# Kernel tuning notes

Hardware: AMD Instinct MI355X
Metric: run time of the kernel (lower is better)

## Reference

```python
import jax, jax.numpy as jnp
import numpy as np

B, N, D = 2, 2048, 1024
H, QH, DH = 8, 16, 64        # kv heads, query heads, head dim
SOFTCLAMP = 50.0


def setup_inputs() -> dict:
    key = jax.random.key(0)
    ks = jax.random.split(key, 7)
    return {
        "tokens": jax.random.normal(ks[0], (B, N, D), jnp.float32),
        "norm_w": jnp.ones((D,), jnp.float32) + 0.02 * jax.random.normal(ks[1], (D,), jnp.float32),
        "Wq":  0.02 * jax.random.normal(ks[2], (D, QH * DH), jnp.float32),
        "Wkv": 0.02 * jax.random.normal(ks[3], (D, 2 * H * DH), jnp.float32),
        "Wout": 0.02 * jax.random.normal(ks[4], (H * DH, D), jnp.float32),
        "q_gamma": 0.02 * jax.random.normal(ks[5], (QH, DH), jnp.float32),
        "k_gamma": 0.02 * jax.random.normal(ks[6], (H, DH), jnp.float32),
    }


def _rmsnorm(x, w):
    eps = jnp.finfo(x.dtype).eps
    return x * jax.lax.rsqrt(jnp.mean(x * x, axis=-1, keepdims=True) + eps) * w


def _l2norm(x):
    # F.normalize(dim=-1, p=2) clamps the norm at eps=1e-12
    n = jnp.maximum(jnp.linalg.norm(x, axis=-1, keepdims=True), 1e-12)
    return x / n


def _mh_rmsnorm(x, gamma):
    # x: [b, h, n, d]; gamma: [h, d]; scale = (gamma + 1) * sqrt(d)
    scale = (gamma + 1.0) * np.sqrt(x.shape[-1]).astype(np.float32)
    return _l2norm(x) * scale[None, :, None, :]


def reference(tokens, norm_w, Wq, Wkv, Wout, q_gamma, k_gamma):
    b, n, d = tokens.shape
    x = _rmsnorm(tokens, norm_w)

    q = (x @ Wq).reshape(b, n, QH, DH).transpose(0, 2, 1, 3)      # [b, QH, n, dh]
    kv = x @ Wkv
    k = kv[..., : H * DH].reshape(b, n, H, DH).transpose(0, 2, 1, 3)  # [b, H, n, dh]
    v = kv[..., H * DH:].reshape(b, n, H, DH).transpose(0, 2, 1, 3)   # [b, H, n, dh]

    q = _mh_rmsnorm(q, q_gamma)
    k = _mh_rmsnorm(k, k_gamma)

    g = QH // H
    q = q.reshape(b, H, g, n, DH)                                 # [b, h, g, i, dh]

    sim = jnp.einsum('bhgid,bhjd->bhgij', q, k)                   # [b, h, g, i, j]
    sim = jnp.tanh(sim / SOFTCLAMP) * SOFTCLAMP                   # softcap BEFORE scale (faithful)
    sim = sim * (DH ** -0.5)

    neg = -jnp.finfo(sim.dtype).max
    causal = jnp.triu(jnp.ones((n, n), dtype=bool), 1)
    sim = jnp.where(causal, neg, sim)

    attn = jax.nn.softmax(sim, axis=-1)
    # NOTE: original einsum sums over the group axis g -> [b, h, i, dh]
    out = jnp.einsum('bhgij,bhjd->bhid', attn, v)
    out = out.transpose(0, 2, 1, 3).reshape(b, n, H * DH)
    return out @ Wout
```

## Files before the change

kernel.cpp:

```cpp
#include <hip/hip_runtime.h>
#include <hip/hip_bf16.h>
#include <type_traits>

typedef unsigned short u16;
typedef __attribute__((ext_vector_type(2))) float f32x2;
typedef __attribute__((ext_vector_type(4))) float f32x4;
typedef __attribute__((ext_vector_type(8))) short short8;
typedef __attribute__((ext_vector_type(4))) short short4v;
typedef __attribute__((ext_vector_type(8))) __bf16 bf16x8;
typedef __attribute__((ext_vector_type(4))) __bf16 bf16x4;

#define BB 2
#define NN 2048
#define DDIM 1024
#define HH 8
#define QHH 16
#define DHH 64

__device__ __forceinline__ float b2f(u16 v) {
    return __builtin_bit_cast(float, ((unsigned)v) << 16);
}
__device__ __forceinline__ u16 f2b(float f) {
    unsigned u = __builtin_bit_cast(unsigned, f);
    u += 0x7FFFu + ((u >> 16) & 1u);
    return (u16)(u >> 16);
}
__device__ __forceinline__ float fastrcp(float x) {
#if __has_builtin(__builtin_amdgcn_rcpf)
    return __builtin_amdgcn_rcpf(x);
#else
    return 1.0f / x;
#endif
}
__device__ __forceinline__ float fastexp2(float x) {
#if __has_builtin(__builtin_amdgcn_exp2f)
    return __builtin_amdgcn_exp2f(x);
#else
    return exp2f(x);
#endif
}
__device__ __forceinline__ f32x2 sp2(float v) { return (f32x2){v, v}; }
__device__ __forceinline__ f32x4 mfma16(short8 a, short8 b, f32x4 c) {
    return __builtin_amdgcn_mfma_f32_16x16x32_bf16(
        __builtin_bit_cast(bf16x8, a), __builtin_bit_cast(bf16x8, b), c, 0, 0, 0);
}
#if __has_builtin(__builtin_amdgcn_mfma_f32_16x16x16_bf16)
__device__ __forceinline__ f32x4 mfma_k16(short4v a, short4v b, f32x4 c) {
    return __builtin_amdgcn_mfma_f32_16x16x16_bf16(
        __builtin_bit_cast(bf16x4, a), __builtin_bit_cast(bf16x4, b), c, 0, 0, 0);
}
#else
__device__ __forceinline__ f32x4 mfma_k16(short4v a, short4v b, f32x4 c) {
    return __builtin_amdgcn_mfma_f32_16x16x16bf16_1k(a, b, c, 0, 0, 0);
}
#endif
__device__ __forceinline__ void stage16(const u16* g, u16* l, int lane) {
#if __has_builtin(__builtin_amdgcn_global_load_lds)
    __builtin_amdgcn_global_load_lds(
        (const __attribute__((address_space(1))) unsigned int*)g,
        (__attribute__((address_space(3))) unsigned int*)l, 16, 0, 0);
#else
    *(short8*)(l + lane * 8) = *(const short8*)g;
#endif
}

__global__ __launch_bounds__(256) void k_rmsnorm(const float* __restrict__ tokens,
                                                 const float* __restrict__ norm_w,
                                                 u16* __restrict__ xb) {
    const int row = blockIdx.x;
    const int tid = threadIdx.x;
    const float* xp = tokens + (size_t)row * DDIM + tid * 4;
    float4 raw = *(const float4*)xp;
    float ss = raw.x * raw.x + raw.y * raw.y + raw.z * raw.z + raw.w * raw.w;
#pragma unroll
    for (int d = 1; d < 64; d <<= 1) ss += __shfl_xor(ss, d);
    __shared__ float red[4];
    if ((tid & 63) == 0) red[tid >> 6] = ss;
    __syncthreads();
    float tot = red[0] + red[1] + red[2] + red[3];
    float r = rsqrtf(tot * (1.0f / 1024.0f) + 1.1920929e-7f);
    float4 wv = *(const float4*)(norm_w + tid * 4);
    ushort4 o;
    o.x = f2b(raw.x * r * wv.x);
    o.y = f2b(raw.y * r * wv.y);
    o.z = f2b(raw.z * r * wv.z);
    o.w = f2b(raw.w * r * wv.w);
    *(ushort4*)(xb + (size_t)row * DDIM + tid * 4) = o;
}

__global__ __launch_bounds__(256) void k_wprep(const float* __restrict__ Wq,
                                               const float* __restrict__ Wkv,
                                               const float* __restrict__ Wout,
                                               u16* __restrict__ WqT,
                                               u16* __restrict__ WkvT,
                                               u16* __restrict__ WoutT) {
    const int z = blockIdx.z;
    const float* in = (z == 0) ? Wq : (z == 1) ? Wkv : Wout;
    u16* out = (z == 0) ? WqT : (z == 1) ? WkvT : WoutT;
    const int R = (z == 2) ? 512 : 1024, C = 1024;
    const int br = blockIdx.y * 32;
    if (br >= R) return;
    __shared__ u16 tile[32][33];
    const int bc = blockIdx.x * 32;
    const int tx = threadIdx.x & 31, ty = threadIdx.x >> 5;
#pragma unroll
    for (int i = 0; i < 32; i += 8) tile[ty + i][tx] = f2b(in[(size_t)(br + ty + i) * C + bc + tx]);
    __syncthreads();
#pragma unroll
    for (int i = 0; i < 32; i += 8) out[(size_t)(bc + ty + i) * R + br + tx] = tile[tx][ty + i];
}

__global__ __launch_bounds__(256) void k_gemm128(const u16* __restrict__ A,
                                                 const u16* __restrict__ Bt,
                                                 u16* __restrict__ C,
                                                 int M, int Ncols, int K) {
    __shared__ __attribute__((aligned(16))) u16 As[128 * 32];
    __shared__ __attribute__((aligned(16))) u16 Bs[128 * 32];
    const int tid = threadIdx.x;
    const int lane = tid & 63;
    const int w = tid >> 6;
    const int m0 = blockIdx.y * 128;
    const int n0 = blockIdx.x * 128;
    const int wr = (w >> 1) * 64;
    const int wc = (w & 1) * 64;
    const int lr = lane & 15;
    const int lq = lane >> 4;

    const int ch0 = w * 32;
    const u16* aSrc = A + (size_t)(m0 + ch0 + (lane >> 2)) * K + (lane & 3) * 8;
    const u16* bSrc = Bt + (size_t)(n0 + ch0 + (lane >> 2)) * K + (lane & 3) * 8;
    u16* aDst = As + ch0 * 32;
    u16* bDst = Bs + ch0 * 32;

    f32x4 acc[4][4];
#pragma unroll
    for (int i = 0; i < 4; i++)
#pragma unroll
        for (int j = 0; j < 4; j++) acc[i][j] = (f32x4){0.f, 0.f, 0.f, 0.f};

    for (int k0 = 0; k0 < K; k0 += 32) {
        __syncthreads();
        stage16(aSrc, aDst, lane);
        stage16(aSrc + (size_t)16 * K, aDst + 512, lane);
        stage16(bSrc, bDst, lane);
        stage16(bSrc + (size_t)16 * K, bDst + 512, lane);
        aSrc += 32;
        bSrc += 32;
        __syncthreads();
        short8 a[4], b[4];
#pragma unroll
        for (int mi = 0; mi < 4; ++mi) a[mi] = *(const short8*)&As[(wr + mi * 16 + lr) * 32 + lq * 8];
#pragma unroll
        for (int ni = 0; ni < 4; ++ni) b[ni] = *(const short8*)&Bs[(wc + ni * 16 + lr) * 32 + lq * 8];
#pragma unroll
        for (int mi = 0; mi < 4; ++mi)
#pragma unroll
            for (int ni = 0; ni < 4; ++ni) acc[mi][ni] = mfma16(a[mi], b[ni], acc[mi][ni]);
    }
#pragma unroll
    for (int mi = 0; mi < 4; ++mi)
#pragma unroll
        for (int ni = 0; ni < 4; ++ni)
#pragma unroll
            for (int r = 0; r < 4; ++r) {
                int row = m0 + wr + mi * 16 + lq * 4 + r;
                int col = n0 + wc + ni * 16 + lr;
                C[(size_t)row * Ncols + col] = f2b(acc[mi][ni][r]);
            }
}

__global__ __launch_bounds__(256) void k_gemm64f(const u16* __restrict__ A,
                                                 const u16* __restrict__ Bt,
                                                 float* __restrict__ C,
                                                 int M, int Ncols, int K) {
    __shared__ __attribute__((aligned(16))) u16 As[64 * 32];
    __shared__ __attribute__((aligned(16))) u16 Bs[128 * 32];
    const int tid = threadIdx.x;
    const int lane = tid & 63;
    const int w = tid >> 6;
    const int m0 = blockIdx.y * 64;
    const int n0 = blockIdx.x * 128;
    const int lr = lane & 15;
    const int lq = lane >> 4;

    const u16* aSrc = A + (size_t)(m0 + w * 16 + (lane >> 2)) * K + (lane & 3) * 8;
    const u16* bSrc = Bt + (size_t)(n0 + w * 32 + (lane >> 2)) * K + (lane & 3) * 8;
    u16* aDst = As + w * 16 * 32;
    u16* bDst = Bs + w * 32 * 32;

    f32x4 acc[8];
#pragma unroll
    for (int i = 0; i < 8; i++) acc[i] = (f32x4){0.f, 0.f, 0.f, 0.f};

    for (int k0 = 0; k0 < K; k0 += 32) {
        __syncthreads();
        stage16(aSrc, aDst, lane);
        stage16(bSrc, bDst, lane);
        stage16(bSrc + (size_t)16 * K, bDst + 512, lane);
        aSrc += 32;
        bSrc += 32;
        __syncthreads();
        short8 a = *(const short8*)&As[(w * 16 + lr) * 32 + lq * 8];
#pragma unroll
        for (int nt = 0; nt < 8; ++nt) {
            short8 b = *(const short8*)&Bs[(nt * 16 + lr) * 32 + lq * 8];
            acc[nt] = mfma16(a, b, acc[nt]);
        }
    }
#pragma unroll
    for (int nt = 0; nt < 8; ++nt)
#pragma unroll
        for (int r = 0; r < 4; ++r) {
            int row = m0 + w * 16 + lq * 4 + r;
            int col = n0 + nt * 16 + lr;
            C[(size_t)row * Ncols + col] = acc[nt][r];
        }
}

__global__ __launch_bounds__(256) void k_headnorm(const u16* __restrict__ qkv,
                                                  const float* __restrict__ q_gamma,
                                                  const float* __restrict__ k_gamma,
                                                  u16* __restrict__ qn,
                                                  u16* __restrict__ kn) {
    const int row = blockIdx.x;
    const int b = row >> 11, n = row & 2047;
    const int lane = threadIdx.x & 63, w = threadIdx.x >> 6;
    const u16* qr = qkv + (size_t)row * 2048;
    const u16* kvr = qkv + (size_t)row * 2048 + 1024;
#pragma unroll
    for (int t = 0; t < 4; ++t) {
        int qh = w * 4 + t;
        float v = b2f(qr[qh * 64 + lane]);
        float ss = v * v;
#pragma unroll
        for (int d = 1; d < 64; d <<= 1) ss += __shfl_xor(ss, d);
        float nrm = fmaxf(sqrtf(ss), 1e-12f);
        float g = q_gamma[qh * 64 + lane];
        qn[((size_t)(b * QHH + qh) * NN + n) * 64 + lane] = f2b(v / nrm * (g + 1.0f) * 8.0f);
    }
#pragma unroll
    for (int t = 0; t < 2; ++t) {
        int kh = w * 2 + t;
        float v = b2f(kvr[kh * 64 + lane]);
        float ss = v * v;
#pragma unroll
        for (int d = 1; d < 64; d <<= 1) ss += __shfl_xor(ss, d);
        float nrm = fmaxf(sqrtf(ss), 1e-12f);
        float g = k_gamma[kh * 64 + lane];
        kn[((size_t)(b * HH + kh) * NN + n) * 64 + lane] = f2b(v / nrm * (g + 1.0f) * 0.16f);
    }
}

__global__ __launch_bounds__(256) void k_vtrans(const u16* __restrict__ qkv,
                                                u16* __restrict__ vt) {
    const int bh = blockIdx.x;
    const int b = bh >> 3, h = bh & 7;
    const int n0 = blockIdx.y * 64;
    const int tid = threadIdx.x;
    __shared__ u16 t[64 * 72];
#pragma unroll
    for (int it = 0; it < 2; ++it) {
        int idx = tid + it * 256;
        int i = idx >> 3, c = idx & 7;
        short8 v = *(const short8*)&qkv[(size_t)(b * NN + n0 + i) * 2048 + 1536 + h * 64 + c * 8];
        *(short8*)&t[i * 72 + c * 8] = v;
    }
    __syncthreads();
#pragma unroll
    for (int it = 0; it < 2; ++it) {
        int idx = tid + it * 256;
        int d = idx >> 3, c = idx & 7;
        const int sw = (d >> 3) & 1;
        u16 tmp[8], o[8];
#pragma unroll
        for (int j = 0; j < 8; ++j) tmp[j] = t[(c * 8 + j) * 72 + d];
#pragma unroll
        for (int j = 0; j < 8; ++j) o[j] = tmp[j ^ (sw << 2)];
        *(short8*)&vt[((size_t)(bh * 64 + d)) * NN + n0 + c * 8] = *(short8*)o;
    }
}

__global__ __launch_bounds__(256) void k_attn(const u16* __restrict__ qn,
                                              const u16* __restrict__ kn,
                                              const u16* __restrict__ vt,
                                              u16* __restrict__ OT,
                                              float* __restrict__ Lp) {
    const int bq = blockIdx.x;
    const int b = bq >> 4, qh = bq & 15;
    const int h = qh >> 1;
    const int tid = threadIdx.x;
    const int lane = tid & 63, w = tid >> 6;
    const int lr = lane & 15, lq = lane >> 4;
    const int y = blockIdx.y;
    const int z = 31 - (y >> 1);
    const int s = y & 1;
    const int ntile = z + 1;
    const int jmid = (ntile + 1) >> 1;
    const int jb = s ? jmid : 0;
    const int je = s ? ntile : jmid;
    const int ntl = je - jb;
    const int i0 = z * 64 + w * 16;
    const int irow = i0 + lr;

    const u16* Qp = qn + (size_t)(b * QHH + qh) * NN * 64;
    const u16* Kp = kn + (size_t)(b * HH + h) * NN * 64;
    const u16* Vp = vt + (size_t)(b * HH + h) * 64 * NN;
    u16* Op = OT + (size_t)s * (BB * QHH * NN * 64) + (size_t)bq * NN * 64;
    float* Lsel = Lp + (size_t)s * (BB * QHH * NN) + (size_t)bq * NN;

    __shared__ __attribute__((aligned(16))) u16 Ks[2][64 * 64];
    __shared__ __attribute__((aligned(16))) u16 Vs[2][64 * 64];

    short8 qf0 = *(const short8*)&Qp[(size_t)(i0 + lr) * 64 + lq * 8];
    short8 qf1 = *(const short8*)&Qp[(size_t)(i0 + lr) * 64 + 32 + lq * 8];

    f32x4 of[4];
#pragma unroll
    for (int dt = 0; dt < 4; ++dt) of[dt] = (f32x4){0.f, 0.f, 0.f, 0.f};
    f32x2 ls = {0.f, 0.f};

    const int srow = lane >> 3;
    const int sch = (lane ^ srow) & 7;
    const int rA = w * 16, rB = w * 16 + 8;

    const u16* kSrcA = Kp + (size_t)jb * 4096 + (size_t)(rA + srow) * 64 + sch * 8;
    const u16* kSrcB = Kp + (size_t)jb * 4096 + (size_t)(rB + srow) * 64 + sch * 8;
    const u16* vSrcA = Vp + (size_t)(rA + srow) * NN + jb * 64 + sch * 8;
    const u16* vSrcB = Vp + (size_t)(rB + srow) * NN + jb * 64 + sch * 8;

    auto stageKV = [&](int buf) {
        stage16(kSrcA, &Ks[buf][rA * 64], lane);
        stage16(kSrcB, &Ks[buf][rB * 64], lane);
        stage16(vSrcA, &Vs[buf][rA * 64], lane);
        stage16(vSrcB, &Vs[buf][rB * 64], lane);
        kSrcA += 64 * 64;
        kSrcB += 64 * 64;
        vSrcA += 64;
        vSrcB += 64;
    };

    auto smax = [&](f32x4 sc, int lim, bool masked) -> short4v {
        f32x2 xa = {sc[0], sc[1]};
        f32x2 xb = {sc[2], sc[3]};
        f32x2 ya = xa * xa;
        f32x2 yb = xb * xb;
        f32x2 Ga = __builtin_elementwise_fma(ya, __builtin_elementwise_fma(ya,
                       __builtin_elementwise_fma(ya, __builtin_elementwise_fma(ya,
                           sp2(0.04705711f), sp2(-0.32327190f)), sp2(1.11500760f)),
                       sp2(-2.98719110f)), sp2(9.01599730f));
        f32x2 Gb = __builtin_elementwise_fma(yb, __builtin_elementwise_fma(yb,
                       __builtin_elementwise_fma(yb, __builtin_elementwise_fma(yb,
                           sp2(0.04705711f), sp2(-0.32327190f)), sp2(1.11500760f)),
                       sp2(-2.98719110f)), sp2(9.01599730f));
        f32x2 aa = __builtin_elementwise_fma(xa, Ga, sp2(-9.0168440f));
        f32x2 ab = __builtin_elementwise_fma(xb, Gb, sp2(-9.0168440f));
        float p0 = fastexp2(aa.x);
        float p1 = fastexp2(aa.y);
        float p2 = fastexp2(ab.x);
        float p3 = fastexp2(ab.y);
        if (masked) {
            p0 = (0 <= lim) ? p0 : 0.0f;
            p1 = (1 <= lim) ? p1 : 0.0f;
            p2 = (2 <= lim) ? p2 : 0.0f;
            p3 = (3 <= lim) ? p3 : 0.0f;
        }
        ls += (f32x2){p0, p1};
        ls += (f32x2){p2, p3};
        bf16x4 pb;
        pb[0] = (__bf16)p0;
        pb[1] = (__bf16)p1;
        pb[2] = (__bf16)p2;
        pb[3] = (__bf16)p3;
        return __builtin_bit_cast(short4v, pb);
    };

    auto tile = [&](int buf, int jt) {
        const int j0 = jt << 6;
        const u16* kb = &Ks[buf][0];
        const u16* vb = &Vs[buf][0];
        f32x4 sc[4];
        __builtin_amdgcn_s_setprio(1);
#pragma unroll
        for (int ct = 0; ct < 4; ++ct) {
            const int r = ct * 16 + lr;
            short8 kf0 = *(const short8*)&kb[r * 64 + ((lq ^ (lr & 7)) << 3)];
            short8 kf1 = *(const short8*)&kb[r * 64 + (((4 + lq) ^ (lr & 7)) << 3)];
            f32x4 t = (f32x4){0.f, 0.f, 0.f, 0.f};
            t = mfma16(kf0, qf0, t);
            t = mfma16(kf1, qf1, t);
            sc[ct] = t;
        }
        __builtin_amdgcn_s_setprio(0);
        const bool masked = (jt == ntile - 1);
        short4v pk[4];
#pragma unroll
        for (int ct = 0; ct < 4; ++ct) {
            const int lim = irow - (j0 + ct * 16 + lq * 4);
            pk[ct] = smax(sc[ct], lim, masked);
        }
        __builtin_amdgcn_s_setprio(1);
#pragma unroll
        for (int dt = 0; dt < 4; ++dt) {
            const int d = dt * 16 + lr;
#pragma unroll
            for (int ct = 0; ct < 4; ++ct) {
                short4v vf = *(const short4v*)
                    &vb[d * 64 + ((((ct << 1) + (lq >> 1)) ^ (lr & 7)) << 3) +
                        (((lq ^ (lr >> 3)) & 1) << 2)];
                of[dt] = mfma_k16(vf, pk[ct], of[dt]);
            }
        }
        __builtin_amdgcn_s_setprio(0);
    };

    if (ntl > 0) {
        stageKV(0);
        for (int t = 0; t < ntl; ++t) {
            const int buf = t & 1;
            __syncthreads();
            if (t + 1 < ntl) stageKV(buf ^ 1);
            tile(buf, jb + t);
        }
    }

    float l = ls.x + ls.y;
    l += __shfl_xor(l, 16);
    l += __shfl_xor(l, 32);
#pragma unroll
    for (int dt = 0; dt < 4; ++dt) {
        u16 o[4];
#pragma unroll
        for (int r = 0; r < 4; ++r) o[r] = f2b(of[dt][r]);
        *(ushort4*)&Op[(size_t)irow * 64 + dt * 16 + lq * 4] = *(ushort4*)o;
    }
    if (lq == 0) Lsel[irow] = l;
}

__global__ __launch_bounds__(256) void k_gsum(const u16* __restrict__ O,
                                              const float* __restrict__ Lp,
                                              u16* __restrict__ AO) {
    const int idx = blockIdx.x * 256 + threadIdx.x;
    const int c8 = idx & 63;
    const int n = (idx >> 6) & 2047;
    const int b = idx >> 17;
    const int hh = c8 >> 3;
    const int ch = c8 & 7;
    const int q0 = b * QHH + 2 * hh, q1 = q0 + 1;
    const size_t SOFF = (size_t)BB * QHH * NN * 64;
    const size_t LOFF = (size_t)BB * QHH * NN;
    const u16* a0 = O + ((size_t)q0 * NN + n) * 64 + ch * 8;
    const u16* a1 = O + ((size_t)q1 * NN + n) * 64 + ch * 8;
    const u16* b0 = a0 + SOFF;
    const u16* b1 = a1 + SOFF;
    const float l0 = Lp[(size_t)q0 * NN + n] + Lp[LOFF + (size_t)q0 * NN + n];
    const float l1 = Lp[(size_t)q1 * NN + n] + Lp[LOFF + (size_t)q1 * NN + n];
    const float inv0 = fastrcp(l0);
    const float inv1 = fastrcp(l1);
    short8 va0 = *(const short8*)a0;
    short8 vb0 = *(const short8*)b0;
    short8 va1 = *(const short8*)a1;
    short8 vb1 = *(const short8*)b1;
    u16 o[8];
#pragma unroll
    for (int j = 0; j < 8; ++j)
        o[j] = f2b((b2f((u16)va0[j]) + b2f((u16)vb0[j])) * inv0 +
                   (b2f((u16)va1[j]) + b2f((u16)vb1[j])) * inv1);
    *(short8*)&AO[((size_t)(b * NN + n)) * 512 + c8 * 8] = *(short8*)o;
}

extern "C" void kernel_launch(void* const* d_in, const int* in_sizes, int n_in,
                              void* d_out, int out_size, void* d_ws, size_t ws_size,
                              hipStream_t stream) {
    const float* tokens = (const float*)d_in[0];
    const float* norm_w = (const float*)d_in[1];
    const float* Wq = (const float*)d_in[2];
    const float* Wkv = (const float*)d_in[3];
    const float* Wout = (const float*)d_in[4];
    const float* q_gamma = (const float*)d_in[5];
    const float* k_gamma = (const float*)d_in[6];
    float* out = (float*)d_out;

    char* ws = (char*)d_ws;
    u16* xb = (u16*)(ws + 0);
    u16* WqT = (u16*)(ws + 8388608);
    u16* WkvT = (u16*)(ws + 10485760);
    u16* WoutT = (u16*)(ws + 12582912);
    u16* qkv = (u16*)(ws + 13631488);
    u16* kn = (u16*)(ws + 30408704);
    u16* vtb = (u16*)(ws + 34603008);
    u16* qn = xb;
    u16* Opart = qkv;
    float* Lpart = (float*)(ws + 8388608);
    u16* AO = kn;

    k_rmsnorm<<<4096, 256, 0, stream>>>(tokens, norm_w, xb);
    k_wprep<<<dim3(32, 32, 3), 256, 0, stream>>>(Wq, Wkv, Wout, WqT, WkvT, WoutT);
    k_gemm128<<<dim3(16, 32), 256, 0, stream>>>(xb, WqT, qkv, 4096, 2048, 1024);
    k_headnorm<<<4096, 256, 0, stream>>>(qkv, q_gamma, k_gamma, qn, kn);
    k_vtrans<<<dim3(16, 32), 256, 0, stream>>>(qkv, vtb);
    k_attn<<<dim3(32, 64), 256, 0, stream>>>(qn, kn, vtb, Opart, Lpart);
    k_gsum<<<1024, 256, 0, stream>>>(Opart, Lpart, AO);
    k_gemm64f<<<dim3(8, 64), 256, 0, stream>>>(AO, WoutT, out, 4096, 1024, 512);
}
```

Baseline: 186.9 us.

## Merge elementwise launches and single-buffer attention K/V staging

Merges rmsnorm with weight preparation, and head-norm with the V transpose, into two combined kernels that pick their role by block index. This cuts the launch count by two. In the attention kernel the double-buffered K/V shared-memory tiles become a single buffer, with a sync before and after each stage. That halves LDS use, which may raise occupancy, but it gives up the overlap of the next tile's load with the current tile's compute.

```diff
diff --git a/kernel.cpp b/kernel.cpp
--- a/kernel.cpp
+++ b/kernel.cpp
@@ -64,50 +64,57 @@
 #endif
 }
 
-__global__ __launch_bounds__(256) void k_rmsnorm(const float* __restrict__ tokens,
-                                                 const float* __restrict__ norm_w,
-                                                 u16* __restrict__ xb) {
-    const int row = blockIdx.x;
+__global__ __launch_bounds__(256) void k_pre(const float* __restrict__ tokens,
+                                             const float* __restrict__ norm_w,
+                                             u16* __restrict__ xb,
+                                             const float* __restrict__ Wq,
+                                             const float* __restrict__ Wkv,
+                                             const float* __restrict__ Wout,
+                                             u16* __restrict__ WqT,
+                                             u16* __restrict__ WkvT,
+                                             u16* __restrict__ WoutT) {
+    __shared__ float red[4];
+    __shared__ u16 tile[32][33];
+    const int bid = blockIdx.x;
     const int tid = threadIdx.x;
-    const float* xp = tokens + (size_t)row * DDIM + tid * 4;
-    float4 raw = *(const float4*)xp;
-    float ss = raw.x * raw.x + raw.y * raw.y + raw.z * raw.z + raw.w * raw.w;
-#pragma unroll
-    for (int d = 1; d < 64; d <<= 1) ss += __shfl_xor(ss, d);
-    __shared__ float red[4];
-    if ((tid & 63) == 0) red[tid >> 6] = ss;
-    __syncthreads();
-    float tot = red[0] + red[1] + red[2] + red[3];
-    float r = rsqrtf(tot * (1.0f / 1024.0f) + 1.1920929e-7f);
-    float4 wv = *(const float4*)(norm_w + tid * 4);
-    ushort4 o;
-    o.x = f2b(raw.x * r * wv.x);
-    o.y = f2b(raw.y * r * wv.y);
-    o.z = f2b(raw.z * r * wv.z);
-    o.w = f2b(raw.w * r * wv.w);
-    *(ushort4*)(xb + (size_t)row * DDIM + tid * 4) = o;
-}
-
-__global__ __launch_bounds__(256) void k_wprep(const float* __restrict__ Wq,
-                                               const float* __restrict__ Wkv,
-                                               const float* __restrict__ Wout,
-                                               u16* __restrict__ WqT,
-                                               u16* __restrict__ WkvT,
-                                               u16* __restrict__ WoutT) {
-    const int z = blockIdx.z;
-    const float* in = (z == 0) ? Wq : (z == 1) ? Wkv : Wout;
-    u16* out = (z == 0) ? WqT : (z == 1) ? WkvT : WoutT;
-    const int R = (z == 2) ? 512 : 1024, C = 1024;
-    const int br = blockIdx.y * 32;
-    if (br >= R) return;
-    __shared__ u16 tile[32][33];
-    const int bc = blockIdx.x * 32;
-    const int tx = threadIdx.x & 31, ty = threadIdx.x >> 5;
-#pragma unroll
-    for (int i = 0; i < 32; i += 8) tile[ty + i][tx] = f2b(in[(size_t)(br + ty + i) * C + bc + tx]);
-    __syncthreads();
-#pragma unroll
-    for (int i = 0; i < 32; i += 8) out[(size_t)(bc + ty + i) * R + br + tx] = tile[tx][ty + i];
+    if (bid < 4096) {
+        const int row = bid;
+        const float* xp = tokens + (size_t)row * DDIM + tid * 4;
+        float4 raw = *(const float4*)xp;
+        float ss = raw.x * raw.x + raw.y * raw.y + raw.z * raw.z + raw.w * raw.w;
+#pragma unroll
+        for (int d = 1; d < 64; d <<= 1) ss += __shfl_xor(ss, d);
+        if ((tid & 63) == 0) red[tid >> 6] = ss;
+        __syncthreads();
+        float tot = red[0] + red[1] + red[2] + red[3];
+        float r = rsqrtf(tot * (1.0f / 1024.0f) + 1.1920929e-7f);
+        float4 wv = *(const float4*)(norm_w + tid * 4);
+        ushort4 o;
+        o.x = f2b(raw.x * r * wv.x);
+        o.y = f2b(raw.y * r * wv.y);
+        o.z = f2b(raw.z * r * wv.z);
+        o.w = f2b(raw.w * r * wv.w);
+        *(ushort4*)(xb + (size_t)row * DDIM + tid * 4) = o;
+    } else {
+        const int idx = bid - 4096;
+        const int z = idx >> 10;
+        const int rem = idx & 1023;
+        const int by = rem >> 5, bx = rem & 31;
+        const float* in = (z == 0) ? Wq : (z == 1) ? Wkv : Wout;
+        u16* out = (z == 0) ? WqT : (z == 1) ? WkvT : WoutT;
+        const int R = (z == 2) ? 512 : 1024, C = 1024;
+        const int br = by * 32;
+        if (br >= R) return;
+        const int bc = bx * 32;
+        const int tx = tid & 31, ty = tid >> 5;
+#pragma unroll
+        for (int i = 0; i < 32; i += 8)
+            tile[ty + i][tx] = f2b(in[(size_t)(br + ty + i) * C + bc + tx]);
+        __syncthreads();
+#pragma unroll
+        for (int i = 0; i < 32; i += 8)
+            out[(size_t)(bc + ty + i) * R + br + tx] = tile[tx][ty + i];
+    }
 }
 
 __global__ __launch_bounds__(256) void k_gemm128(const u16* __restrict__ A,
@@ -217,66 +224,68 @@
         }
 }
 
-__global__ __launch_bounds__(256) void k_headnorm(const u16* __restrict__ qkv,
-                                                  const float* __restrict__ q_gamma,
-                                                  const float* __restrict__ k_gamma,
-                                                  u16* __restrict__ qn,
-                                                  u16* __restrict__ kn) {
-    const int row = blockIdx.x;
-    const int b = row >> 11, n = row & 2047;
-    const int lane = threadIdx.x & 63, w = threadIdx.x >> 6;
-    const u16* qr = qkv + (size_t)row * 2048;
-    const u16* kvr = qkv + (size_t)row * 2048 + 1024;
-#pragma unroll
-    for (int t = 0; t < 4; ++t) {
-        int qh = w * 4 + t;
-        float v = b2f(qr[qh * 64 + lane]);
-        float ss = v * v;
-#pragma unroll
-        for (int d = 1; d < 64; d <<= 1) ss += __shfl_xor(ss, d);
-        float nrm = fmaxf(sqrtf(ss), 1e-12f);
-        float g = q_gamma[qh * 64 + lane];
-        qn[((size_t)(b * QHH + qh) * NN + n) * 64 + lane] = f2b(v / nrm * (g + 1.0f) * 8.0f);
-    }
-#pragma unroll
-    for (int t = 0; t < 2; ++t) {
-        int kh = w * 2 + t;
-        float v = b2f(kvr[kh * 64 + lane]);
-        float ss = v * v;
-#pragma unroll
-        for (int d = 1; d < 64; d <<= 1) ss += __shfl_xor(ss, d);
-        float nrm = fmaxf(sqrtf(ss), 1e-12f);
-        float g = k_gamma[kh * 64 + lane];
-        kn[((size_t)(b * HH + kh) * NN + n) * 64 + lane] = f2b(v / nrm * (g + 1.0f) * 0.16f);
-    }
-}
-
-__global__ __launch_bounds__(256) void k_vtrans(const u16* __restrict__ qkv,
-                                                u16* __restrict__ vt) {
-    const int bh = blockIdx.x;
-    const int b = bh >> 3, h = bh & 7;
-    const int n0 = blockIdx.y * 64;
+__global__ __launch_bounds__(256) void k_mid(const u16* __restrict__ qkv,
+                                             const float* __restrict__ q_gamma,
+                                             const float* __restrict__ k_gamma,
+                                             u16* __restrict__ qn,
+                                             u16* __restrict__ kn,
+                                             u16* __restrict__ vt) {
+    __shared__ u16 t[64 * 72];
+    const int bid = blockIdx.x;
     const int tid = threadIdx.x;
-    __shared__ u16 t[64 * 72];
-#pragma unroll
-    for (int it = 0; it < 2; ++it) {
-        int idx = tid + it * 256;
-        int i = idx >> 3, c = idx & 7;
-        short8 v = *(const short8*)&qkv[(size_t)(b * NN + n0 + i) * 2048 + 1536 + h * 64 + c * 8];
-        *(short8*)&t[i * 72 + c * 8] = v;
-    }
-    __syncthreads();
-#pragma unroll
-    for (int it = 0; it < 2; ++it) {
-        int idx = tid + it * 256;
-        int d = idx >> 3, c = idx & 7;
-        const int sw = (d >> 3) & 1;
-        u16 tmp[8], o[8];
-#pragma unroll
-        for (int j = 0; j < 8; ++j) tmp[j] = t[(c * 8 + j) * 72 + d];
-#pragma unroll
-        for (int j = 0; j < 8; ++j) o[j] = tmp[j ^ (sw << 2)];
-        *(short8*)&vt[((size_t)(bh * 64 + d)) * NN + n0 + c * 8] = *(short8*)o;
+    if (bid < 4096) {
+        const int row = bid;
+        const int b = row >> 11, n = row & 2047;
+        const int lane = tid & 63, w = tid >> 6;
+        const u16* qr = qkv + (size_t)row * 2048;
+        const u16* kvr = qkv + (size_t)row * 2048 + 1024;
+#pragma unroll
+        for (int tq = 0; tq < 4; ++tq) {
+            int qh = w * 4 + tq;
+            float v = b2f(qr[qh * 64 + lane]);
+            float ss = v * v;
+#pragma unroll
+            for (int d = 1; d < 64; d <<= 1) ss += __shfl_xor(ss, d);
+            float nrm = fmaxf(sqrtf(ss), 1e-12f);
+            float g = q_gamma[qh * 64 + lane];
+            qn[((size_t)(b * QHH + qh) * NN + n) * 64 + lane] = f2b(v / nrm * (g + 1.0f) * 8.0f);
+        }
+#pragma unroll
+        for (int tk = 0; tk < 2; ++tk) {
+            int kh = w * 2 + tk;
+            float v = b2f(kvr[kh * 64 + lane]);
+            float ss = v * v;
+#pragma unroll
+            for (int d = 1; d < 64; d <<= 1) ss += __shfl_xor(ss, d);
+            float nrm = fmaxf(sqrtf(ss), 1e-12f);
+            float g = k_gamma[kh * 64 + lane];
+            kn[((size_t)(b * HH + kh) * NN + n) * 64 + lane] = f2b(v / nrm * (g + 1.0f) * 0.16f);
+        }
+    } else {
+        const int idx = bid - 4096;
+        const int bh = idx & 15;
+        const int b = bh >> 3, h = bh & 7;
+        const int n0 = (idx >> 4) * 64;
+#pragma unroll
+        for (int it = 0; it < 2; ++it) {
+            int id2 = tid + it * 256;
+            int i = id2 >> 3, c = id2 & 7;
+            short8 v = *(const short8*)&qkv[(size_t)(b * NN + n0 + i) * 2048 + 1536 + h * 64 + c * 8];
+            *(short8*)&t[i * 72 + c * 8] = v;
+        }
+        __syncthreads();
+#pragma unroll
+        for (int it = 0; it < 2; ++it) {
+            int id2 = tid + it * 256;
+            int d = id2 >> 3, c = id2 & 7;
+            const int sw = (d >> 3) & 1;
+            u16 tmp[8], o[8];
+#pragma unroll
+            for (int j = 0; j < 8; ++j) tmp[j] = t[(c * 8 + j) * 72 + d];
+#pragma unroll
+            for (int j = 0; j < 8; ++j) o[j] = tmp[j ^ (sw << 2)];
+            *(short8*)&vt[((size_t)(bh * 64 + d)) * NN + n0 + c * 8] = *(short8*)o;
+        }
     }
 }
 
@@ -308,8 +317,8 @@
     u16* Op = OT + (size_t)s * (BB * QHH * NN * 64) + (size_t)bq * NN * 64;
     float* Lsel = Lp + (size_t)s * (BB * QHH * NN) + (size_t)bq * NN;
 
-    __shared__ __attribute__((aligned(16))) u16 Ks[2][64 * 64];
-    __shared__ __attribute__((aligned(16))) u16 Vs[2][64 * 64];
+    __shared__ __attribute__((aligned(16))) u16 Ks[64 * 64];
+    __shared__ __attribute__((aligned(16))) u16 Vs[64 * 64];
 
     short8 qf0 = *(const short8*)&Qp[(size_t)(i0 + lr) * 64 + lq * 8];
     short8 qf1 = *(const short8*)&Qp[(size_t)(i0 + lr) * 64 + 32 + lq * 8];
@@ -328,11 +337,11 @@
     const u16* vSrcA = Vp + (size_t)(rA + srow) * NN + jb * 64 + sch * 8;
     const u16* vSrcB = Vp + (size_t)(rB + srow) * NN + jb * 64 + sch * 8;
 
-    auto stageKV = [&](int buf) {
-        stage16(kSrcA, &Ks[buf][rA * 64], lane);
-        stage16(kSrcB, &Ks[buf][rB * 64], lane);
-        stage16(vSrcA, &Vs[buf][rA * 64], lane);
-        stage16(vSrcB, &Vs[buf][rB * 64], lane);
+    auto stageKV = [&]() {
+        stage16(kSrcA, &Ks[rA * 64], lane);
+        stage16(kSrcB, &Ks[rB * 64], lane);
+        stage16(vSrcA, &Vs[rA * 64], lane);
+        stage16(vSrcB, &Vs[rB * 64], lane);
         kSrcA += 64 * 64;
         kSrcB += 64 * 64;
         vSrcA += 64;
@@ -374,10 +383,10 @@
         return __builtin_bit_cast(short4v, pb);
     };
 
-    auto tile = [&](int buf, int jt) {
+    auto tile = [&](int jt) {
         const int j0 = jt << 6;
-        const u16* kb = &Ks[buf][0];
-        const u16* vb = &Vs[buf][0];
+        const u16* kb = &Ks[0];
+        const u16* vb = &Vs[0];
         f32x4 sc[4];
         __builtin_amdgcn_s_setprio(1);
 #pragma unroll
@@ -413,14 +422,11 @@
         __builtin_amdgcn_s_setprio(0);
     };
 
-    if (ntl > 0) {
-        stageKV(0);
-        for (int t = 0; t < ntl; ++t) {
-            const int buf = t & 1;
-            __syncthreads();
-            if (t + 1 < ntl) stageKV(buf ^ 1);
-            tile(buf, jb + t);
-        }
+    for (int t = 0; t < ntl; ++t) {
+        __syncthreads();
+        stageKV();
+        __syncthreads();
+        tile(jb + t);
     }
 
     float l = ls.x + ls.y;
@@ -493,11 +499,9 @@
     float* Lpart = (float*)(ws + 8388608);
     u16* AO = kn;
 
-    k_rmsnorm<<<4096, 256, 0, stream>>>(tokens, norm_w, xb);
-    k_wprep<<<dim3(32, 32, 3), 256, 0, stream>>>(Wq, Wkv, Wout, WqT, WkvT, WoutT);
+    k_pre<<<7168, 256, 0, stream>>>(tokens, norm_w, xb, Wq, Wkv, Wout, WqT, WkvT, WoutT);
     k_gemm128<<<dim3(16, 32), 256, 0, stream>>>(xb, WqT, qkv, 4096, 2048, 1024);
-    k_headnorm<<<4096, 256, 0, stream>>>(qkv, q_gamma, k_gamma, qn, kn);
-    k_vtrans<<<dim3(16, 32), 256, 0, stream>>>(qkv, vtb);
+    k_mid<<<4608, 256, 0, stream>>>(qkv, q_gamma, k_gamma, qn, kn, vtb);
     k_attn<<<dim3(32, 64), 256, 0, stream>>>(qn, kn, vtb, Opart, Lpart);
     k_gsum<<<1024, 256, 0, stream>>>(Opart, Lpart, AO);
     k_gemm64f<<<dim3(8, 64), 256, 0, stream>>>(AO, WoutT, out, 4096, 1024, 512);
```

After: 180.3 us. -3.6%, faster.
